# Optimization experiments

Hardware: AMD Instinct MI355X
Metric: run time of the kernel (lower is better)

## Reference

```python
import jax, jax.numpy as jnp
import numpy as np

B, S, D_IN, D_OUT = 4, 2048, 1024, 1024

def setup_inputs() -> dict:
    key = jax.random.key(0)
    k_x, k_q, k_k, k_v = jax.random.split(key, 4)
    return {
        "x": jax.random.normal(k_x, (B, S, D_IN), dtype=jnp.float32),
        "W_query": jax.random.uniform(k_q, (D_IN, D_OUT), dtype=jnp.float32),
        "W_key": jax.random.uniform(k_k, (D_IN, D_OUT), dtype=jnp.float32),
        "W_value": jax.random.uniform(k_v, (D_IN, D_OUT), dtype=jnp.float32),
    }

def reference(x, W_query, W_key, W_value):
    seq_len = x.shape[1]
    d_out = W_key.shape[-1]
    # fused QKV projection: x @ concat([Wq, Wk, Wv], -1), then split
    qkv = x @ jnp.concatenate([W_query, W_key, W_value], axis=-1)  # [B,S,3*d_out]
    query, key, value = jnp.split(qkv, 3, axis=2)
    # raw scores [B,S,S]; causal mask applied BEFORE scaling (as in source)
    attn_weights = jnp.einsum("bqd,bkd->bqk", query, key)
    causal = jnp.triu(jnp.ones((seq_len, seq_len), dtype=bool), k=1)
    attn_weights = jnp.where(causal[None, :, :], -jnp.inf, attn_weights)
    scaled = attn_weights / jnp.asarray(d_out, x.dtype) ** 0.5
    attn_scores = jax.nn.softmax(scaled, axis=-1)  # dropout p=0 -> identity
    context_vectors = jnp.einsum("bqk,bkd->bqd", attn_scores, value)
    return (context_vectors, attn_scores)
```

## Files before the change

### kernel.cpp

```cpp
#include <hip/hip_runtime.h>
#include <cstdint>
#include <cstddef>


#define S_LEN 2048
#define D_DIM 1024
#define NBATCH 4
#define MEG (1024 * 1024)

typedef __attribute__((ext_vector_type(4))) float floatx4;
typedef __attribute__((ext_vector_type(8))) __bf16 bf16x8;
typedef __attribute__((ext_vector_type(8))) short short8v;

__device__ __forceinline__ unsigned short f2bf(float f) {
  union { float f; unsigned u; } v; v.f = f;
  unsigned r = v.u + 0x7FFF + ((v.u >> 16) & 1);
  return (unsigned short)(r >> 16);
}
__device__ __forceinline__ float bf2f(unsigned short h) {
  union { unsigned u; float f; } v; v.u = ((unsigned)h) << 16; return v.f;
}

__device__ __forceinline__ void async_copy16(const void* g, void* l) {
  __builtin_amdgcn_global_load_lds(
      (const __attribute__((address_space(1))) void*)g,
      (__attribute__((address_space(3))) void*)l, 16, 0, 0);
}

#define VMCNT0() asm volatile("s_waitcnt vmcnt(0)" ::: "memory")
#define RAW_BAR() __builtin_amdgcn_s_barrier()
#define MFMA_BF16 __builtin_amdgcn_mfma_f32_16x16x32_bf16


__device__ __forceinline__ void split_core8_db(
    const short* __restrict__ Ah, const short* __restrict__ Al,
    const short* __restrict__ Bh, const short* __restrict__ Bl,
    int lda, int ldb, int kIters, int blockM, int blockN,
    short (*AsH)[256][32], short (*AsL)[256][32],
    short (*BsH)[128][32], short (*BsL)[128][32],
    floatx4 (&acc)[4][4])
{
  const int tid  = threadIdx.x;
  const int lane = tid & 63;
  const int wave = tid >> 6;
  const int wm = (wave >> 1) * 64;
  const int wn = (wave & 1) * 64;
  const int fm = lane & 15;
  const int fu = lane >> 4;

  int rA[4], sA[4], rB[4], sB[4];
  #pragma unroll
  for (int i = 0; i < 4; ++i) {
    rA[i] = wm + i * 16 + fm;
    sA[i] = (fu ^ ((rA[i] >> 1) & 3)) * 8;
    rB[i] = wn + i * 16 + fm;
    sB[i] = (fu ^ ((rB[i] >> 1) & 3)) * 8;
  }

  floatx4 zero = {0.f, 0.f, 0.f, 0.f};
  #pragma unroll
  for (int i = 0; i < 4; ++i)
    #pragma unroll
    for (int j = 0; j < 4; ++j)
      acc[i][j] = zero;

  const int r0 = tid >> 2;
  const int u0 = tid & 3;
  const int su = (u0 ^ ((r0 >> 1) & 3)) * 8;
  const size_t a0 = (size_t)(blockM + r0) * lda + su;
  const size_t a1 = a0 + (size_t)128 * lda;
  const size_t b0 = (size_t)(blockN + r0) * ldb + su;

  auto stage0 = [&](int bf, int kb) {
    async_copy16(Ah + a0 + kb, &AsH[bf][r0][u0 * 8]);
    async_copy16(Al + a0 + kb, &AsL[bf][r0][u0 * 8]);
    async_copy16(Bh + b0 + kb, &BsH[bf][r0][u0 * 8]);
  };
  auto stage1 = [&](int bf, int kb) {
    async_copy16(Ah + a1 + kb, &AsH[bf][r0 + 128][u0 * 8]);
    async_copy16(Al + a1 + kb, &AsL[bf][r0 + 128][u0 * 8]);
    async_copy16(Bl + b0 + kb, &BsL[bf][r0][u0 * 8]);
  };

  stage0(0, 0);
  stage1(0, 0);
  VMCNT0();
  RAW_BAR();

  for (int kt = 0; kt < kIters; ++kt) {
    const int cur = kt & 1;
    const int kb = (kt + 1) * 32;
    const bool pf = (kt + 1) < kIters;

    bf16x8 bh[4], bl[4];
    #pragma unroll
    for (int j = 0; j < 4; ++j) {
      bh[j] = *(const bf16x8*)(&BsH[cur][rB[j]][sB[j]]);
      bl[j] = *(const bf16x8*)(&BsL[cur][rB[j]][sB[j]]);
    }
    bf16x8 ah0 = *(const bf16x8*)(&AsH[cur][rA[0]][sA[0]]);
    bf16x8 al0 = *(const bf16x8*)(&AsL[cur][rA[0]][sA[0]]);
    bf16x8 ah1 = *(const bf16x8*)(&AsH[cur][rA[1]][sA[1]]);
    bf16x8 al1 = *(const bf16x8*)(&AsL[cur][rA[1]][sA[1]]);
    if (pf) stage0(cur ^ 1, kb);
    RAW_BAR();
    __builtin_amdgcn_s_setprio(1);
    #pragma unroll
    for (int j = 0; j < 4; ++j) {
      acc[0][j] = MFMA_BF16(ah0, bh[j], acc[0][j], 0, 0, 0);
      acc[0][j] = MFMA_BF16(ah0, bl[j], acc[0][j], 0, 0, 0);
      acc[0][j] = MFMA_BF16(al0, bh[j], acc[0][j], 0, 0, 0);
      acc[1][j] = MFMA_BF16(ah1, bh[j], acc[1][j], 0, 0, 0);
      acc[1][j] = MFMA_BF16(ah1, bl[j], acc[1][j], 0, 0, 0);
      acc[1][j] = MFMA_BF16(al1, bh[j], acc[1][j], 0, 0, 0);
    }
    __builtin_amdgcn_s_setprio(0);
    RAW_BAR();

    bf16x8 ah2 = *(const bf16x8*)(&AsH[cur][rA[2]][sA[2]]);
    bf16x8 al2 = *(const bf16x8*)(&AsL[cur][rA[2]][sA[2]]);
    bf16x8 ah3 = *(const bf16x8*)(&AsH[cur][rA[3]][sA[3]]);
    bf16x8 al3 = *(const bf16x8*)(&AsL[cur][rA[3]][sA[3]]);
    if (pf) stage1(cur ^ 1, kb);
    RAW_BAR();
    __builtin_amdgcn_s_setprio(1);
    #pragma unroll
    for (int j = 0; j < 4; ++j) {
      acc[2][j] = MFMA_BF16(ah2, bh[j], acc[2][j], 0, 0, 0);
      acc[2][j] = MFMA_BF16(ah2, bl[j], acc[2][j], 0, 0, 0);
      acc[2][j] = MFMA_BF16(al2, bh[j], acc[2][j], 0, 0, 0);
      acc[3][j] = MFMA_BF16(ah3, bh[j], acc[3][j], 0, 0, 0);
      acc[3][j] = MFMA_BF16(ah3, bl[j], acc[3][j], 0, 0, 0);
      acc[3][j] = MFMA_BF16(al3, bh[j], acc[3][j], 0, 0, 0);
    }
    __builtin_amdgcn_s_setprio(0);
    VMCNT0();
    RAW_BAR();
  }
}

__device__ __forceinline__ void split_core8_sb(
    const short* __restrict__ Ah, const short* __restrict__ Al,
    const short* __restrict__ Bh, const short* __restrict__ Bl,
    int lda, int ldb, int kIters, int blockM, int blockN,
    short (*AsH)[32], short (*AsL)[32],
    short (*BsH)[32], short (*BsL)[32],
    floatx4 (&acc)[4][4])
{
  const int tid  = threadIdx.x;
  const int lane = tid & 63;
  const int wave = tid >> 6;
  const int wm = (wave >> 1) * 64;
  const int wn = (wave & 1) * 64;
  const int fm = lane & 15;
  const int fu = lane >> 4;

  int rA[4], sA[4], rB[4], sB[4];
  #pragma unroll
  for (int i = 0; i < 4; ++i) {
    rA[i] = wm + i * 16 + fm;
    sA[i] = (fu ^ ((rA[i] >> 1) & 3)) * 8;
    rB[i] = wn + i * 16 + fm;
    sB[i] = (fu ^ ((rB[i] >> 1) & 3)) * 8;
  }

  floatx4 zero = {0.f, 0.f, 0.f, 0.f};
  #pragma unroll
  for (int i = 0; i < 4; ++i)
    #pragma unroll
    for (int j = 0; j < 4; ++j)
      acc[i][j] = zero;

  const int r0 = tid >> 2;
  const int u0 = tid & 3;
  const int su = (u0 ^ ((r0 >> 1) & 3)) * 8;
  const size_t a0 = (size_t)(blockM + r0) * lda + su;
  const size_t a1 = a0 + (size_t)128 * lda;
  const size_t b0 = (size_t)(blockN + r0) * ldb + su;

  for (int kt = 0; kt < kIters; ++kt) {
    const int kb = kt * 32;
    async_copy16(Ah + a0 + kb, &AsH[r0][u0 * 8]);
    async_copy16(Al + a0 + kb, &AsL[r0][u0 * 8]);
    async_copy16(Bh + b0 + kb, &BsH[r0][u0 * 8]);
    async_copy16(Ah + a1 + kb, &AsH[r0 + 128][u0 * 8]);
    async_copy16(Al + a1 + kb, &AsL[r0 + 128][u0 * 8]);
    async_copy16(Bl + b0 + kb, &BsL[r0][u0 * 8]);
    __syncthreads();

    bf16x8 bh[4], bl[4], ah[4], al[4];
    #pragma unroll
    for (int j = 0; j < 4; ++j) {
      bh[j] = *(const bf16x8*)(&BsH[rB[j]][sB[j]]);
      bl[j] = *(const bf16x8*)(&BsL[rB[j]][sB[j]]);
    }
    #pragma unroll
    for (int i = 0; i < 4; ++i) {
      ah[i] = *(const bf16x8*)(&AsH[rA[i]][sA[i]]);
      al[i] = *(const bf16x8*)(&AsL[rA[i]][sA[i]]);
    }
    __builtin_amdgcn_s_setprio(1);
    #pragma unroll
    for (int i = 0; i < 4; ++i)
      #pragma unroll
      for (int j = 0; j < 4; ++j) {
        acc[i][j] = MFMA_BF16(ah[i], bh[j], acc[i][j], 0, 0, 0);
        acc[i][j] = MFMA_BF16(ah[i], bl[j], acc[i][j], 0, 0, 0);
        acc[i][j] = MFMA_BF16(al[i], bh[j], acc[i][j], 0, 0, 0);
      }
    __builtin_amdgcn_s_setprio(0);
    __syncthreads();
  }
}

__device__ __forceinline__ void single_core8_sb(
    const short* __restrict__ A, const short* __restrict__ B,
    int lda, int ldb, int kIters, int blockM, int blockN,
    short (*As)[32], short (*Bs)[32], floatx4 (&acc)[4][4])
{
  const int tid  = threadIdx.x;
  const int lane = tid & 63;
  const int wave = tid >> 6;
  const int wm = (wave >> 1) * 64;
  const int wn = (wave & 1) * 64;
  const int fm = lane & 15;
  const int fu = lane >> 4;

  int rA[4], sA[4], rB[4], sB[4];
  #pragma unroll
  for (int i = 0; i < 4; ++i) {
    rA[i] = wm + i * 16 + fm;
    sA[i] = (fu ^ ((rA[i] >> 1) & 3)) * 8;
    rB[i] = wn + i * 16 + fm;
    sB[i] = (fu ^ ((rB[i] >> 1) & 3)) * 8;
  }

  floatx4 zero = {0.f, 0.f, 0.f, 0.f};
  #pragma unroll
  for (int i = 0; i < 4; ++i)
    #pragma unroll
    for (int j = 0; j < 4; ++j)
      acc[i][j] = zero;

  const int r0 = tid >> 2;
  const int u0 = tid & 3;
  const int su = (u0 ^ ((r0 >> 1) & 3)) * 8;
  const size_t a0 = (size_t)(blockM + r0) * lda + su;
  const size_t a1 = a0 + (size_t)128 * lda;
  const size_t b0 = (size_t)(blockN + r0) * ldb + su;

  for (int kt = 0; kt < kIters; ++kt) {
    const int kb = kt * 32;
    async_copy16(A + a0 + kb, &As[r0][u0 * 8]);
    async_copy16(B + b0 + kb, &Bs[r0][u0 * 8]);
    async_copy16(A + a1 + kb, &As[r0 + 128][u0 * 8]);
    __syncthreads();

    bf16x8 bfr[4], af[4];
    #pragma unroll
    for (int j = 0; j < 4; ++j)
      bfr[j] = *(const bf16x8*)(&Bs[rB[j]][sB[j]]);
    #pragma unroll
    for (int i = 0; i < 4; ++i)
      af[i] = *(const bf16x8*)(&As[rA[i]][sA[i]]);

    __builtin_amdgcn_s_setprio(1);
    #pragma unroll
    for (int i = 0; i < 4; ++i)
      #pragma unroll
      for (int j = 0; j < 4; ++j)
        acc[i][j] = MFMA_BF16(af[i], bfr[j], acc[i][j], 0, 0, 0);
    __builtin_amdgcn_s_setprio(0);
    __syncthreads();
  }
}


__global__ __launch_bounds__(256) void k_cvt_w(
    const float* __restrict__ wq, const float* __restrict__ wk,
    const float* __restrict__ wv,
    short* __restrict__ wqh, short* __restrict__ wql,
    short* __restrict__ wkh, short* __restrict__ wkl,
    short* __restrict__ wvt, float* __restrict__ muSum,
    int* __restrict__ cnt)
{
  const int bid = blockIdx.x;
  const int tid = threadIdx.x;
  if (bid < 1024) {
    const float4* src;
    short *dh, *dl;
    size_t idx;
    if (bid < 512) {
      idx = (size_t)bid * 256 + tid;
      src = (const float4*)wq; dh = wqh; dl = wql;
    } else {
      idx = (size_t)(bid - 512) * 256 + tid;
      src = (const float4*)wk; dh = wkh; dl = wkl;
    }
    const float4 u4 = src[idx * 2];
    const float4 w4 = src[idx * 2 + 1];
    float f[8] = {u4.x, u4.y, u4.z, u4.w, w4.x, w4.y, w4.z, w4.w};
    short8v oh, ol;
    #pragma unroll
    for (int e = 0; e < 8; ++e) {
      const unsigned short h = f2bf(f[e]);
      oh[e] = (short)h;
      ol[e] = (short)f2bf(f[e] - bf2f(h));
    }
    *(short8v*)(dh + idx * 8) = oh;
    *(short8v*)(dl + idx * 8) = ol;
  } else {
    if (bid == 1024) {
      float4 z = {0.f, 0.f, 0.f, 0.f};
      ((float4*)muSum)[tid] = z;
      if (tid == 0) *cnt = 0;
    }
    const int rem = bid - 1024;
    const int bx = rem & 31, by = rem >> 5;
    const int tx = tid & 31, ty = tid >> 5;
    __shared__ float tile[32][33];
    const int colIn = bx * 32 + tx;
    #pragma unroll
    for (int i = 0; i < 4; ++i) {
      const int rowIn = by * 32 + ty + i * 8;
      tile[ty + i * 8][tx] = wv[(size_t)rowIn * D_DIM + colIn];
    }
    __syncthreads();
    const int colOut = by * 32 + tx;
    #pragma unroll
    for (int i = 0; i < 4; ++i) {
      const int rowOut = bx * 32 + ty + i * 8;
      wvt[(size_t)rowOut * D_DIM + colOut] = (short)f2bf(tile[tx][ty + i * 8]);
    }
  }
}


__global__ __launch_bounds__(256) void k_m_cvtx(
    const short* __restrict__ wqh, const short* __restrict__ wql,
    const short* __restrict__ wkh, const short* __restrict__ wkl,
    short* __restrict__ mth, short* __restrict__ mtl,
    float* __restrict__ muSum,
    const float4* __restrict__ x,
    short* __restrict__ xh, short* __restrict__ xl)
{
  __shared__ alignas(16) short AsH[2][64][32];
  __shared__ alignas(16) short AsL[2][64][32];
  __shared__ alignas(16) short BsH[2][64][32];
  __shared__ alignas(16) short BsL[2][64][32];
  const int g = blockIdx.x;
  const int tid = threadIdx.x;

  if (g < 256) {
    floatx4 acc[2][2];
    const int blockM = (g >> 4) * 64;
    const int blockN = (g & 15) * 64;
    const int lane = tid & 63, wave = tid >> 6;
    const int wm = (wave >> 1) * 32, wn = (wave & 1) * 32;
    const int fm = lane & 15, fk = (lane >> 4) * 8;

    floatx4 zero = {0.f, 0.f, 0.f, 0.f};
    #pragma unroll
    for (int i = 0; i < 2; ++i)
      #pragma unroll
      for (int j = 0; j < 2; ++j)
        acc[i][j] = zero;

    const int sr = tid >> 2;
    const int sc = (tid & 3) * 8;
    const short* ah0 = wkh + (size_t)(blockM + sr) * D_DIM + sc;
    const short* al0 = wkl + (size_t)(blockM + sr) * D_DIM + sc;
    const short* bh0 = wqh + (size_t)(blockN + sr) * D_DIM + sc;
    const short* bl0 = wql + (size_t)(blockN + sr) * D_DIM + sc;
    short* ahB = &AsH[0][0][0]; short* alB = &AsL[0][0][0];
    short* bhB = &BsH[0][0][0]; short* blB = &BsL[0][0][0];
    const int l0 = tid * 8, l1 = (tid + 256) * 8;

    for (int kt = 0; kt < 16; ++kt) {
      const int kb = kt * 64;
      async_copy16(ah0 + kb, ahB + l0);
      async_copy16(ah0 + kb + 32, ahB + l1);
      async_copy16(al0 + kb, alB + l0);
      async_copy16(al0 + kb + 32, alB + l1);
      async_copy16(bh0 + kb, bhB + l0);
      async_copy16(bh0 + kb + 32, bhB + l1);
      async_copy16(bl0 + kb, blB + l0);
      async_copy16(bl0 + kb + 32, blB + l1);
      __syncthreads();
      #pragma unroll
      for (int ks = 0; ks < 2; ++ks) {
        bf16x8 ah[2], al[2], bh[2], bl[2];
        #pragma unroll
        for (int i = 0; i < 2; ++i) {
          ah[i] = *(const bf16x8*)(&AsH[ks][wm + i * 16 + fm][fk]);
          al[i] = *(const bf16x8*)(&AsL[ks][wm + i * 16 + fm][fk]);
        }
        #pragma unroll
        for (int j = 0; j < 2; ++j) {
          bh[j] = *(const bf16x8*)(&BsH[ks][wn + j * 16 + fm][fk]);
          bl[j] = *(const bf16x8*)(&BsL[ks][wn + j * 16 + fm][fk]);
        }
        #pragma unroll
        for (int i = 0; i < 2; ++i)
          #pragma unroll
          for (int j = 0; j < 2; ++j) {
            acc[i][j] = MFMA_BF16(ah[i], bh[j], acc[i][j], 0, 0, 0);
            acc[i][j] = MFMA_BF16(ah[i], bl[j], acc[i][j], 0, 0, 0);
            acc[i][j] = MFMA_BF16(al[i], bh[j], acc[i][j], 0, 0, 0);
          }
      }
      __syncthreads();
    }

    const int rb = wm + ((lane >> 4) << 2);
    const int cb = wn + (lane & 15);
    #pragma unroll
    for (int i = 0; i < 2; ++i)
      #pragma unroll
      for (int j = 0; j < 2; ++j) {
        const int n = blockN + cb + j * 16;
        #pragma unroll
        for (int r = 0; r < 2 * 2; ++r) {
          const int m = blockM + rb + i * 16 + r;
          const float f = acc[i][j][r];
          const unsigned short h = f2bf(f);
          mth[(size_t)m * D_DIM + n] = (short)h;
          mtl[(size_t)m * D_DIM + n] = (short)f2bf(f - bf2f(h));
        }
      }
    #pragma unroll
    for (int i = 0; i < 2; ++i)
      #pragma unroll
      for (int r = 0; r < 4; ++r) {
        float v = acc[i][0][r] + acc[i][1][r];
        v += __shfl_xor(v, 1); v += __shfl_xor(v, 2);
        v += __shfl_xor(v, 4); v += __shfl_xor(v, 8);
        if ((lane & 15) == 0)
          atomicAdd(&muSum[blockM + rb + i * 16 + r], v);
      }
  } else {
    const size_t idx = (size_t)(g - 256) * 256 + tid;
    const float4 u4 = x[idx * 2];
    const float4 w4 = x[idx * 2 + 1];
    float f[8] = {u4.x, u4.y, u4.z, u4.w, w4.x, w4.y, w4.z, w4.w};
    short8v oh, ol;
    #pragma unroll
    for (int e = 0; e < 8; ++e) {
      const unsigned short h = f2bf(f[e]);
      oh[e] = (short)h;
      ol[e] = (short)f2bf(f[e] - bf2f(h));
    }
    *(short8v*)(xh + idx * 8) = oh;
    *(short8v*)(xl + idx * 8) = ol;
  }
}


__global__ __launch_bounds__(256) void k_rowstats(
    const short* __restrict__ xh, const short* __restrict__ xl,
    const float* __restrict__ muSum, float* __restrict__ sq, float* __restrict__ u)
{
  const int r = blockIdx.x, tid = threadIdx.x;
  const ushort4 h = *(const ushort4*)(xh + (size_t)r * D_DIM + tid * 4);
  const ushort4 l = *(const ushort4*)(xl + (size_t)r * D_DIM + tid * 4);
  const float4 m4 = *(const float4*)(muSum + tid * 4);
  const float x0 = bf2f(h.x) + bf2f(l.x);
  const float x1 = bf2f(h.y) + bf2f(l.y);
  const float x2 = bf2f(h.z) + bf2f(l.z);
  const float x3 = bf2f(h.w) + bf2f(l.w);
  float s = x0 + x1 + x2 + x3;
  float uu = m4.x * x0 + m4.y * x1 + m4.z * x2 + m4.w * x3;
  #pragma unroll
  for (int off = 32; off > 0; off >>= 1) {
    s  += __shfl_xor(s, off);
    uu += __shfl_xor(uu, off);
  }
  __shared__ float ps[4], pu[4];
  if ((tid & 63) == 0) { ps[tid >> 6] = s; pu[tid >> 6] = uu; }
  __syncthreads();
  if (tid == 0) {
    sq[r] = ps[0] + ps[1] + ps[2] + ps[3];
    u[r]  = (pu[0] + pu[1] + pu[2] + pu[3]) * (1.0f / 1024.0f);
  }
}


__global__ __launch_bounds__(512) void k_gemm_n8(
    const short* __restrict__ xh, const short* __restrict__ xl,
    const short* __restrict__ mth, const short* __restrict__ mtl,
    const float* __restrict__ sq, const float* __restrict__ muSum,
    short* __restrict__ nh, short* __restrict__ nl)
{
  __shared__ alignas(16) short AsH[2][256][32];
  __shared__ alignas(16) short AsL[2][256][32];
  __shared__ alignas(16) short BsH[2][128][32];
  __shared__ alignas(16) short BsL[2][128][32];
  floatx4 acc[4][4];
  const int g = blockIdx.x;
  const int swz = (g & 7) * 32 + (g >> 3);
  const int blockM = (swz >> 3) * 256;
  const int blockN = (swz & 7) * 128;
  split_core8_db(xh, xl, mth, mtl, D_DIM, D_DIM, D_DIM / 32,
                 blockM, blockN, AsH, AsL, BsH, BsL, acc);

  const int tid = threadIdx.x, lane = tid & 63, wave = tid >> 6;
  const int wm = (wave >> 1) * 64, wn = (wave & 1) * 64;
  const int rb = wm + ((lane >> 4) << 2);
  const int cb = wn + (lane & 15);
  #pragma unroll
  for (int i = 0; i < 4; ++i)
    #pragma unroll
    for (int j = 0; j < 4; ++j) {
      const int n = blockN + cb + j * 16;
      const float muv = muSum[n] * (1.0f / 1024.0f);
      #pragma unroll
      for (int r = 0; r < 4; ++r) {
        const int m = blockM + rb + i * 16 + r;
        const float f = acc[i][j][r] - sq[m] * muv;
        const unsigned short h = f2bf(f);
        nh[(size_t)m * D_DIM + n] = (short)h;
        nl[(size_t)m * D_DIM + n] = (short)f2bf(f - bf2f(h));
      }
    }
}


__global__ __launch_bounds__(512) void k_gemm_sv8(
    const short* __restrict__ nh, const short* __restrict__ nl,
    const short* __restrict__ xh, const short* __restrict__ xl,
    const float* __restrict__ sq, const float* __restrict__ u,
    const short* __restrict__ wvt, float* __restrict__ attn,
    short* __restrict__ vt, int* __restrict__ cnt)
{
  __shared__ alignas(16) short AsH[256][32];
  __shared__ alignas(16) short AsL[256][32];
  __shared__ alignas(16) short BsH[128][32];
  __shared__ alignas(16) short BsL[128][32];
  __shared__ int s_item;

  const int tid = threadIdx.x, lane = tid & 63, wave = tid >> 6;
  const int wm = (wave >> 1) * 64, wn = (wave & 1) * 64;
  const int rb = wm + ((lane >> 4) << 2);
  const int cb = wn + (lane & 15);

  for (;;) {
    if (tid == 0) s_item = atomicAdd(cnt, 1);
    __syncthreads();
    const int item = s_item;
    if (item >= 544) return;

    floatx4 acc[4][4];
    if (item < 288) {
      const int b = item / 72;
      int t = item - b * 72;
      int bi = 0;
      while (t >= 2 * bi + 2) { t -= 2 * bi + 2; ++bi; }
      const int bj = t;

      const size_t boff = (size_t)b * S_LEN * D_DIM;
      split_core8_sb(nh + boff, nl + boff, xh + boff, xl + boff,
                     D_DIM, D_DIM, D_DIM / 32, bi * 256, bj * 128,
                     AsH, AsL, BsH, BsL, acc);

      float* out = attn + (size_t)b * S_LEN * S_LEN;
      const int rowBase = (b << 11) + bi * 256;
      const int colBase = (b << 11) + bj * 128;
      #pragma unroll
      for (int j = 0; j < 4; ++j) {
        const int n = bj * 128 + cb + j * 16;
        const float uv = u[colBase + cb + j * 16];
        #pragma unroll
        for (int i = 0; i < 4; ++i)
          #pragma unroll
          for (int r = 0; r < 4; ++r) {
            const int m = bi * 256 + rb + i * 16 + r;
            const float sv = sq[rowBase + rb + i * 16 + r];
            out[(size_t)m * S_LEN + n] = acc[i][j][r] + sv * uv;
          }
      }
    } else {
      const int vb = item - 288;
      const int blockM = (vb >> 3) * 256;
      const int blockN = (vb & 7) * 128;
      single_core8_sb(xh, wvt, D_DIM, D_DIM, D_DIM / 32, blockM, blockN,
                      AsH, BsH, acc);
      #pragma unroll
      for (int i = 0; i < 4; ++i)
        #pragma unroll
        for (int j = 0; j < 4; ++j) {
          const int n = blockN + cb + j * 16;
          const int m0 = blockM + rb + i * 16;
          const int b = m0 >> 11;
          const int s0 = m0 & (S_LEN - 1);
          ushort4 pk;
          pk.x = f2bf(acc[i][j][0]); pk.y = f2bf(acc[i][j][1]);
          pk.z = f2bf(acc[i][j][2]); pk.w = f2bf(acc[i][j][3]);
          *(ushort4*)(vt + ((size_t)b * D_DIM + n) * S_LEN + s0) = pk;
        }
    }
  }
}


__global__ __launch_bounds__(256) void k_softmax(float* __restrict__ attn,
                                                 short* __restrict__ pb) {
  const int b = blockIdx.x >> 11;
  const int q = blockIdx.x & (S_LEN - 1);
  float* row  = attn + ((size_t)b * S_LEN + q) * S_LEN;
  short* prow = pb   + ((size_t)b * S_LEN + q) * S_LEN;
  const int tid = threadIdx.x;
  const int k0 = tid * 8;
  const int kBand = ((q >> 7) + 1) << 7;
  __shared__ float sMax[4], sSum[4];

  float v[8];
  if (k0 <= q) {
    const float4 a0 = *(const float4*)(row + k0);
    const float4 a1 = *(const float4*)(row + k0 + 4);
    v[0] = a0.x; v[1] = a0.y; v[2] = a0.z; v[3] = a0.w;
    v[4] = a1.x; v[5] = a1.y; v[6] = a1.z; v[7] = a1.w;
  } else {
    #pragma unroll
    for (int e = 0; e < 8; ++e) v[e] = -3.0e38f;
  }

  float mx = -3.0e38f;
  #pragma unroll
  for (int e = 0; e < 8; ++e) {
    v[e] = (k0 + e <= q) ? v[e] : -3.0e38f;
    mx = fmaxf(mx, v[e]);
  }
  #pragma unroll
  for (int off = 32; off > 0; off >>= 1) mx = fmaxf(mx, __shfl_xor(mx, off));
  if ((tid & 63) == 0) sMax[tid >> 6] = mx;
  __syncthreads();
  mx = fmaxf(fmaxf(sMax[0], sMax[1]), fmaxf(sMax[2], sMax[3]));

  float s = 0.f;
  #pragma unroll
  for (int e = 0; e < 8; ++e) {
    const float p = (k0 + e <= q) ? __expf((v[e] - mx) * 0.03125f) : 0.f;
    v[e] = p;
    s += p;
  }
  #pragma unroll
  for (int off = 32; off > 0; off >>= 1) s += __shfl_xor(s, off);
  if ((tid & 63) == 0) sSum[tid >> 6] = s;
  __syncthreads();
  s = sSum[0] + sSum[1] + sSum[2] + sSum[3];
  const float inv = 1.0f / s;

  float o[8];
  #pragma unroll
  for (int e = 0; e < 8; ++e) o[e] = v[e] * inv;
  float4 w0 = {o[0], o[1], o[2], o[3]};
  float4 w1 = {o[4], o[5], o[6], o[7]};
  *(float4*)(row + k0) = w0;
  *(float4*)(row + k0 + 4) = w1;
  if (k0 < kBand) {
    ushort4 p0, p1;
    p0.x = f2bf(o[0]); p0.y = f2bf(o[1]); p0.z = f2bf(o[2]); p0.w = f2bf(o[3]);
    p1.x = f2bf(o[4]); p1.y = f2bf(o[5]); p1.z = f2bf(o[6]); p1.w = f2bf(o[7]);
    *(ushort4*)(prow + k0) = p0;
    *(ushort4*)(prow + k0 + 4) = p1;
  }
}


__global__ __launch_bounds__(256) void k_gemm_ctx(
    const short* __restrict__ pb, const short* __restrict__ vt,
    float* __restrict__ ctx)
{
  __shared__ alignas(16) short As2[2][128][32];
  __shared__ alignas(16) short Bs2[2][128][32];
  floatx4 acc[4][4];
  const int b = blockIdx.z;
  const int by = 15 - blockIdx.y;
  const int blockM = by * 128;
  const int blockN = blockIdx.x * 128;
  const int kIters = (by + 1) * 2;
  const short* A = pb + (size_t)b * S_LEN * S_LEN;
  const short* B = vt + (size_t)b * D_DIM * S_LEN;

  const int tid = threadIdx.x, lane = tid & 63, wave = tid >> 6;
  const int wm = (wave >> 1) * 64, wn = (wave & 1) * 64;
  const int fm = lane & 15, fk = (lane >> 4) * 8;
  const int r0 = tid >> 2, c0 = (tid & 3) * 8;

  floatx4 zero = {0.f, 0.f, 0.f, 0.f};
  #pragma unroll
  for (int i = 0; i < 4; ++i)
    #pragma unroll
    for (int j = 0; j < 4; ++j)
      acc[i][j] = zero;

  const short* a0 = A + (size_t)(blockM + r0) * S_LEN + c0;
  const short* a1 = a0 + (size_t)64 * S_LEN;
  const short* b0 = B + (size_t)(blockN + r0) * S_LEN + c0;
  const short* b1 = b0 + (size_t)64 * S_LEN;
  short* asBase = &As2[0][0][0];
  short* bsBase = &Bs2[0][0][0];
  short* as0 = asBase + (size_t)tid * 8;
  short* as1 = asBase + (size_t)(tid + 256) * 8;
  short* as2 = asBase + (size_t)(tid + 512) * 8;
  short* as3 = asBase + (size_t)(tid + 768) * 8;
  short* bs0 = bsBase + (size_t)tid * 8;
  short* bs1 = bsBase + (size_t)(tid + 256) * 8;
  short* bs2 = bsBase + (size_t)(tid + 512) * 8;
  short* bs3 = bsBase + (size_t)(tid + 768) * 8;

  for (int kt = 0; kt < kIters; ++kt) {
    const int kb = kt * 64;
    async_copy16(a0 + kb, as0);
    async_copy16(a1 + kb, as1);
    async_copy16(a0 + kb + 32, as2);
    async_copy16(a1 + kb + 32, as3);
    async_copy16(b0 + kb, bs0);
    async_copy16(b1 + kb, bs1);
    async_copy16(b0 + kb + 32, bs2);
    async_copy16(b1 + kb + 32, bs3);
    __syncthreads();
    #pragma unroll
    for (int ks = 0; ks < 2; ++ks) {
      bf16x8 af[4], bfr[4];
      #pragma unroll
      for (int i = 0; i < 4; ++i)
        af[i] = *(const bf16x8*)(&As2[ks][wm + i * 16 + fm][fk]);
      #pragma unroll
      for (int j = 0; j < 4; ++j)
        bfr[j] = *(const bf16x8*)(&Bs2[ks][wn + j * 16 + fm][fk]);
      #pragma unroll
      for (int i = 0; i < 4; ++i)
        #pragma unroll
        for (int j = 0; j < 4; ++j)
          acc[i][j] = MFMA_BF16(af[i], bfr[j], acc[i][j], 0, 0, 0);
    }
    __syncthreads();
  }

  float* out = ctx + (size_t)b * S_LEN * D_DIM;
  const int rb = wm + ((lane >> 4) << 2);
  const int cb = wn + (lane & 15);
  #pragma unroll
  for (int i = 0; i < 4; ++i)
    #pragma unroll
    for (int j = 0; j < 4; ++j) {
      const int n = blockN + cb + j * 16;
      #pragma unroll
      for (int r = 0; r < 4; ++r) {
        const int m = blockM + rb + i * 16 + r;
        out[(size_t)m * D_DIM + n] = acc[i][j][r];
      }
    }
}


extern "C" void kernel_launch(void* const* d_in, const int* in_sizes, int n_in,
                              void* d_out, int out_size, void* d_ws, size_t ws_size,
                              hipStream_t stream) {
  const float* x  = (const float*)d_in[0];
  const float* wq = (const float*)d_in[1];
  const float* wk = (const float*)d_in[2];
  const float* wv = (const float*)d_in[3];

  float* out  = (float*)d_out;
  float* ctx  = out;
  float* attn = out + (size_t)NBATCH * S_LEN * D_DIM;

  short* ws  = (short*)d_ws;
  short* xh  = ws;
  short* xl  = xh + (size_t)8 * MEG;
  short* wqh = xl + (size_t)8 * MEG;
  short* wql = wqh + (size_t)1 * MEG;
  short* wkh = wql + (size_t)1 * MEG;
  short* wkl = wkh + (size_t)1 * MEG;
  short* wvt = wkl + (size_t)1 * MEG;
  short* mth = wvt + (size_t)1 * MEG;
  short* mtl = mth + (size_t)1 * MEG;
  short* nh  = mtl + (size_t)1 * MEG;
  short* nl  = nh + (size_t)8 * MEG;
  short* vt  = nl + (size_t)8 * MEG;
  short* pb  = nh;
  float* fb  = (float*)(vt + (size_t)8 * MEG);
  float* muS = fb;
  float* sq  = fb + 1024;
  float* u   = sq + 8192;
  int*   cnt = (int*)(u + 8192);

  k_cvt_w<<<2048, 256, 0, stream>>>(wq, wk, wv, wqh, wql, wkh, wkl, wvt,
                                    muS, cnt);
  k_m_cvtx<<<4352, 256, 0, stream>>>(wqh, wql, wkh, wkl, mth, mtl, muS,
                                     (const float4*)x, xh, xl);
  k_rowstats<<<8192, 256, 0, stream>>>(xh, xl, muS, sq, u);
  k_gemm_n8<<<256, 512, 0, stream>>>(xh, xl, mth, mtl, sq, muS, nh, nl);
  k_gemm_sv8<<<512, 512, 0, stream>>>(nh, nl, xh, xl, sq, u, wvt, attn,
                                      vt, cnt);
  k_softmax<<<NBATCH * S_LEN, 256, 0, stream>>>(attn, pb);
  k_gemm_ctx<<<dim3(8, 16, 4), 256, 0, stream>>>(pb, vt, ctx);
}
```

Measured before the change: 376.4 us.

## Shrink split-bf16 GEMM tiles to 128x128 with 256-thread blocks and swizzle ctx LDS

The split-precision GEMM kernels move from 256x128 tiles on 512-thread blocks (one of them double-buffered) to 128x128 tiles on 256-thread single-buffered blocks with launch_bounds occupancy 3. The item counts and grids are rescaled so the causal-triangle scheduler covers finer tiles. This gives more blocks and better load balance on the causal triangle, at the cost of less operand reuse per tile and the loss of double buffering. The ctx GEMM also gains an XOR-swizzled LDS layout to cut bank conflicts, plus setprio around its MFMA blocks.

```diff
diff --git a/kernel.cpp b/kernel.cpp
--- a/kernel.cpp
+++ b/kernel.cpp
@@ -32,114 +32,7 @@
 #define MFMA_BF16 __builtin_amdgcn_mfma_f32_16x16x32_bf16
 
 
-__device__ __forceinline__ void split_core8_db(
-    const short* __restrict__ Ah, const short* __restrict__ Al,
-    const short* __restrict__ Bh, const short* __restrict__ Bl,
-    int lda, int ldb, int kIters, int blockM, int blockN,
-    short (*AsH)[256][32], short (*AsL)[256][32],
-    short (*BsH)[128][32], short (*BsL)[128][32],
-    floatx4 (&acc)[4][4])
-{
-  const int tid  = threadIdx.x;
-  const int lane = tid & 63;
-  const int wave = tid >> 6;
-  const int wm = (wave >> 1) * 64;
-  const int wn = (wave & 1) * 64;
-  const int fm = lane & 15;
-  const int fu = lane >> 4;
-
-  int rA[4], sA[4], rB[4], sB[4];
-  #pragma unroll
-  for (int i = 0; i < 4; ++i) {
-    rA[i] = wm + i * 16 + fm;
-    sA[i] = (fu ^ ((rA[i] >> 1) & 3)) * 8;
-    rB[i] = wn + i * 16 + fm;
-    sB[i] = (fu ^ ((rB[i] >> 1) & 3)) * 8;
-  }
-
-  floatx4 zero = {0.f, 0.f, 0.f, 0.f};
-  #pragma unroll
-  for (int i = 0; i < 4; ++i)
-    #pragma unroll
-    for (int j = 0; j < 4; ++j)
-      acc[i][j] = zero;
-
-  const int r0 = tid >> 2;
-  const int u0 = tid & 3;
-  const int su = (u0 ^ ((r0 >> 1) & 3)) * 8;
-  const size_t a0 = (size_t)(blockM + r0) * lda + su;
-  const size_t a1 = a0 + (size_t)128 * lda;
-  const size_t b0 = (size_t)(blockN + r0) * ldb + su;
-
-  auto stage0 = [&](int bf, int kb) {
-    async_copy16(Ah + a0 + kb, &AsH[bf][r0][u0 * 8]);
-    async_copy16(Al + a0 + kb, &AsL[bf][r0][u0 * 8]);
-    async_copy16(Bh + b0 + kb, &BsH[bf][r0][u0 * 8]);
-  };
-  auto stage1 = [&](int bf, int kb) {
-    async_copy16(Ah + a1 + kb, &AsH[bf][r0 + 128][u0 * 8]);
-    async_copy16(Al + a1 + kb, &AsL[bf][r0 + 128][u0 * 8]);
-    async_copy16(Bl + b0 + kb, &BsL[bf][r0][u0 * 8]);
-  };
-
-  stage0(0, 0);
-  stage1(0, 0);
-  VMCNT0();
-  RAW_BAR();
-
-  for (int kt = 0; kt < kIters; ++kt) {
-    const int cur = kt & 1;
-    const int kb = (kt + 1) * 32;
-    const bool pf = (kt + 1) < kIters;
-
-    bf16x8 bh[4], bl[4];
-    #pragma unroll
-    for (int j = 0; j < 4; ++j) {
-      bh[j] = *(const bf16x8*)(&BsH[cur][rB[j]][sB[j]]);
-      bl[j] = *(const bf16x8*)(&BsL[cur][rB[j]][sB[j]]);
-    }
-    bf16x8 ah0 = *(const bf16x8*)(&AsH[cur][rA[0]][sA[0]]);
-    bf16x8 al0 = *(const bf16x8*)(&AsL[cur][rA[0]][sA[0]]);
-    bf16x8 ah1 = *(const bf16x8*)(&AsH[cur][rA[1]][sA[1]]);
-    bf16x8 al1 = *(const bf16x8*)(&AsL[cur][rA[1]][sA[1]]);
-    if (pf) stage0(cur ^ 1, kb);
-    RAW_BAR();
-    __builtin_amdgcn_s_setprio(1);
-    #pragma unroll
-    for (int j = 0; j < 4; ++j) {
-      acc[0][j] = MFMA_BF16(ah0, bh[j], acc[0][j], 0, 0, 0);
-      acc[0][j] = MFMA_BF16(ah0, bl[j], acc[0][j], 0, 0, 0);
-      acc[0][j] = MFMA_BF16(al0, bh[j], acc[0][j], 0, 0, 0);
-      acc[1][j] = MFMA_BF16(ah1, bh[j], acc[1][j], 0, 0, 0);
-      acc[1][j] = MFMA_BF16(ah1, bl[j], acc[1][j], 0, 0, 0);
-      acc[1][j] = MFMA_BF16(al1, bh[j], acc[1][j], 0, 0, 0);
-    }
-    __builtin_amdgcn_s_setprio(0);
-    RAW_BAR();
-
-    bf16x8 ah2 = *(const bf16x8*)(&AsH[cur][rA[2]][sA[2]]);
-    bf16x8 al2 = *(const bf16x8*)(&AsL[cur][rA[2]][sA[2]]);
-    bf16x8 ah3 = *(const bf16x8*)(&AsH[cur][rA[3]][sA[3]]);
-    bf16x8 al3 = *(const bf16x8*)(&AsL[cur][rA[3]][sA[3]]);
-    if (pf) stage1(cur ^ 1, kb);
-    RAW_BAR();
-    __builtin_amdgcn_s_setprio(1);
-    #pragma unroll
-    for (int j = 0; j < 4; ++j) {
-      acc[2][j] = MFMA_BF16(ah2, bh[j], acc[2][j], 0, 0, 0);
-      acc[2][j] = MFMA_BF16(ah2, bl[j], acc[2][j], 0, 0, 0);
-      acc[2][j] = MFMA_BF16(al2, bh[j], acc[2][j], 0, 0, 0);
-      acc[3][j] = MFMA_BF16(ah3, bh[j], acc[3][j], 0, 0, 0);
-      acc[3][j] = MFMA_BF16(ah3, bl[j], acc[3][j], 0, 0, 0);
-      acc[3][j] = MFMA_BF16(al3, bh[j], acc[3][j], 0, 0, 0);
-    }
-    __builtin_amdgcn_s_setprio(0);
-    VMCNT0();
-    RAW_BAR();
-  }
-}
-
-__device__ __forceinline__ void split_core8_sb(
+__device__ __forceinline__ void split_core4(
     const short* __restrict__ Ah, const short* __restrict__ Al,
     const short* __restrict__ Bh, const short* __restrict__ Bl,
     int lda, int ldb, int kIters, int blockM, int blockN,
@@ -175,17 +68,20 @@
   const int u0 = tid & 3;
   const int su = (u0 ^ ((r0 >> 1) & 3)) * 8;
   const size_t a0 = (size_t)(blockM + r0) * lda + su;
-  const size_t a1 = a0 + (size_t)128 * lda;
+  const size_t a1 = a0 + (size_t)64 * lda;
   const size_t b0 = (size_t)(blockN + r0) * ldb + su;
+  const size_t b1 = b0 + (size_t)64 * ldb;
 
   for (int kt = 0; kt < kIters; ++kt) {
     const int kb = kt * 32;
     async_copy16(Ah + a0 + kb, &AsH[r0][u0 * 8]);
+    async_copy16(Ah + a1 + kb, &AsH[r0 + 64][u0 * 8]);
     async_copy16(Al + a0 + kb, &AsL[r0][u0 * 8]);
+    async_copy16(Al + a1 + kb, &AsL[r0 + 64][u0 * 8]);
     async_copy16(Bh + b0 + kb, &BsH[r0][u0 * 8]);
-    async_copy16(Ah + a1 + kb, &AsH[r0 + 128][u0 * 8]);
-    async_copy16(Al + a1 + kb, &AsL[r0 + 128][u0 * 8]);
+    async_copy16(Bh + b1 + kb, &BsH[r0 + 64][u0 * 8]);
     async_copy16(Bl + b0 + kb, &BsL[r0][u0 * 8]);
+    async_copy16(Bl + b1 + kb, &BsL[r0 + 64][u0 * 8]);
     __syncthreads();
 
     bf16x8 bh[4], bl[4], ah[4], al[4];
@@ -213,7 +109,7 @@
   }
 }
 
-__device__ __forceinline__ void single_core8_sb(
+__device__ __forceinline__ void single_core4(
     const short* __restrict__ A, const short* __restrict__ B,
     int lda, int ldb, int kIters, int blockM, int blockN,
     short (*As)[32], short (*Bs)[32], floatx4 (&acc)[4][4])
@@ -246,14 +142,16 @@
   const int u0 = tid & 3;
   const int su = (u0 ^ ((r0 >> 1) & 3)) * 8;
   const size_t a0 = (size_t)(blockM + r0) * lda + su;
-  const size_t a1 = a0 + (size_t)128 * lda;
+  const size_t a1 = a0 + (size_t)64 * lda;
   const size_t b0 = (size_t)(blockN + r0) * ldb + su;
+  const size_t b1 = b0 + (size_t)64 * ldb;
 
   for (int kt = 0; kt < kIters; ++kt) {
     const int kb = kt * 32;
     async_copy16(A + a0 + kb, &As[r0][u0 * 8]);
+    async_copy16(A + a1 + kb, &As[r0 + 64][u0 * 8]);
     async_copy16(B + b0 + kb, &Bs[r0][u0 * 8]);
-    async_copy16(A + a1 + kb, &As[r0 + 128][u0 * 8]);
+    async_copy16(B + b1 + kb, &Bs[r0 + 64][u0 * 8]);
     __syncthreads();
 
     bf16x8 bfr[4], af[4];
@@ -485,23 +383,23 @@
 }
 
 
-__global__ __launch_bounds__(512) void k_gemm_n8(
+__global__ __launch_bounds__(256, 3) void k_gemm_n4(
     const short* __restrict__ xh, const short* __restrict__ xl,
     const short* __restrict__ mth, const short* __restrict__ mtl,
     const float* __restrict__ sq, const float* __restrict__ muSum,
     short* __restrict__ nh, short* __restrict__ nl)
 {
-  __shared__ alignas(16) short AsH[2][256][32];
-  __shared__ alignas(16) short AsL[2][256][32];
-  __shared__ alignas(16) short BsH[2][128][32];
-  __shared__ alignas(16) short BsL[2][128][32];
+  __shared__ alignas(16) short AsH[128][32];
+  __shared__ alignas(16) short AsL[128][32];
+  __shared__ alignas(16) short BsH[128][32];
+  __shared__ alignas(16) short BsL[128][32];
   floatx4 acc[4][4];
   const int g = blockIdx.x;
-  const int swz = (g & 7) * 32 + (g >> 3);
-  const int blockM = (swz >> 3) * 256;
+  const int swz = (g & 7) * 64 + (g >> 3);
+  const int blockM = (swz >> 3) * 128;
   const int blockN = (swz & 7) * 128;
-  split_core8_db(xh, xl, mth, mtl, D_DIM, D_DIM, D_DIM / 32,
-                 blockM, blockN, AsH, AsL, BsH, BsL, acc);
+  split_core4(xh, xl, mth, mtl, D_DIM, D_DIM, D_DIM / 32,
+              blockM, blockN, AsH, AsL, BsH, BsL, acc);
 
   const int tid = threadIdx.x, lane = tid & 63, wave = tid >> 6;
   const int wm = (wave >> 1) * 64, wn = (wave & 1) * 64;
@@ -525,15 +423,15 @@
 }
 
 
-__global__ __launch_bounds__(512) void k_gemm_sv8(
+__global__ __launch_bounds__(256, 3) void k_gemm_sv4(
     const short* __restrict__ nh, const short* __restrict__ nl,
     const short* __restrict__ xh, const short* __restrict__ xl,
     const float* __restrict__ sq, const float* __restrict__ u,
     const short* __restrict__ wvt, float* __restrict__ attn,
     short* __restrict__ vt, int* __restrict__ cnt)
 {
-  __shared__ alignas(16) short AsH[256][32];
-  __shared__ alignas(16) short AsL[256][32];
+  __shared__ alignas(16) short AsH[128][32];
+  __shared__ alignas(16) short AsL[128][32];
   __shared__ alignas(16) short BsH[128][32];
   __shared__ alignas(16) short BsL[128][32];
   __shared__ int s_item;
@@ -547,23 +445,23 @@
     if (tid == 0) s_item = atomicAdd(cnt, 1);
     __syncthreads();
     const int item = s_item;
-    if (item >= 544) return;
+    if (item >= 1056) return;
 
     floatx4 acc[4][4];
-    if (item < 288) {
-      const int b = item / 72;
-      int t = item - b * 72;
+    if (item < 544) {
+      const int b = item / 136;
+      int t = item - b * 136;
       int bi = 0;
-      while (t >= 2 * bi + 2) { t -= 2 * bi + 2; ++bi; }
+      while (t >= bi + 1) { t -= bi + 1; ++bi; }
       const int bj = t;
 
       const size_t boff = (size_t)b * S_LEN * D_DIM;
-      split_core8_sb(nh + boff, nl + boff, xh + boff, xl + boff,
-                     D_DIM, D_DIM, D_DIM / 32, bi * 256, bj * 128,
-                     AsH, AsL, BsH, BsL, acc);
+      split_core4(nh + boff, nl + boff, xh + boff, xl + boff,
+                  D_DIM, D_DIM, D_DIM / 32, bi * 128, bj * 128,
+                  AsH, AsL, BsH, BsL, acc);
 
       float* out = attn + (size_t)b * S_LEN * S_LEN;
-      const int rowBase = (b << 11) + bi * 256;
+      const int rowBase = (b << 11) + bi * 128;
       const int colBase = (b << 11) + bj * 128;
       #pragma unroll
       for (int j = 0; j < 4; ++j) {
@@ -573,17 +471,17 @@
         for (int i = 0; i < 4; ++i)
           #pragma unroll
           for (int r = 0; r < 4; ++r) {
-            const int m = bi * 256 + rb + i * 16 + r;
+            const int m = bi * 128 + rb + i * 16 + r;
             const float sv = sq[rowBase + rb + i * 16 + r];
             out[(size_t)m * S_LEN + n] = acc[i][j][r] + sv * uv;
           }
       }
     } else {
-      const int vb = item - 288;
-      const int blockM = (vb >> 3) * 256;
+      const int vb = item - 544;
+      const int blockM = (vb >> 3) * 128;
       const int blockN = (vb & 7) * 128;
-      single_core8_sb(xh, wvt, D_DIM, D_DIM, D_DIM / 32, blockM, blockN,
-                      AsH, BsH, acc);
+      single_core4(xh, wvt, D_DIM, D_DIM, D_DIM / 32, blockM, blockN,
+                   AsH, BsH, acc);
       #pragma unroll
       for (int i = 0; i < 4; ++i)
         #pragma unroll
@@ -684,8 +582,17 @@
 
   const int tid = threadIdx.x, lane = tid & 63, wave = tid >> 6;
   const int wm = (wave >> 1) * 64, wn = (wave & 1) * 64;
-  const int fm = lane & 15, fk = (lane >> 4) * 8;
-  const int r0 = tid >> 2, c0 = (tid & 3) * 8;
+  const int fm = lane & 15;
+  const int fu = lane >> 4;
+
+  int rA[4], sA[4], rB[4], sB[4];
+  #pragma unroll
+  for (int i = 0; i < 4; ++i) {
+    rA[i] = wm + i * 16 + fm;
+    sA[i] = (fu ^ ((rA[i] >> 1) & 3)) * 8;
+    rB[i] = wn + i * 16 + fm;
+    sB[i] = (fu ^ ((rB[i] >> 1) & 3)) * 8;
+  }
 
   floatx4 zero = {0.f, 0.f, 0.f, 0.f};
   #pragma unroll
@@ -694,9 +601,12 @@
     for (int j = 0; j < 4; ++j)
       acc[i][j] = zero;
 
-  const short* a0 = A + (size_t)(blockM + r0) * S_LEN + c0;
+  const int r0 = tid >> 2;
+  const int u0 = tid & 3;
+  const int su = (u0 ^ ((r0 >> 1) & 3)) * 8;
+  const short* a0 = A + (size_t)(blockM + r0) * S_LEN + su;
   const short* a1 = a0 + (size_t)64 * S_LEN;
-  const short* b0 = B + (size_t)(blockN + r0) * S_LEN + c0;
+  const short* b0 = B + (size_t)(blockN + r0) * S_LEN + su;
   const short* b1 = b0 + (size_t)64 * S_LEN;
   short* asBase = &As2[0][0][0];
   short* bsBase = &Bs2[0][0][0];
@@ -725,15 +635,17 @@
       bf16x8 af[4], bfr[4];
       #pragma unroll
       for (int i = 0; i < 4; ++i)
-        af[i] = *(const bf16x8*)(&As2[ks][wm + i * 16 + fm][fk]);
+        af[i] = *(const bf16x8*)(&As2[ks][rA[i]][sA[i]]);
       #pragma unroll
       for (int j = 0; j < 4; ++j)
-        bfr[j] = *(const bf16x8*)(&Bs2[ks][wn + j * 16 + fm][fk]);
+        bfr[j] = *(const bf16x8*)(&Bs2[ks][rB[j]][sB[j]]);
+      __builtin_amdgcn_s_setprio(1);
       #pragma unroll
       for (int i = 0; i < 4; ++i)
         #pragma unroll
         for (int j = 0; j < 4; ++j)
           acc[i][j] = MFMA_BF16(af[i], bfr[j], acc[i][j], 0, 0, 0);
+      __builtin_amdgcn_s_setprio(0);
     }
     __syncthreads();
   }
@@ -792,8 +704,8 @@
   k_m_cvtx<<<4352, 256, 0, stream>>>(wqh, wql, wkh, wkl, mth, mtl, muS,
                                      (const float4*)x, xh, xl);
   k_rowstats<<<8192, 256, 0, stream>>>(xh, xl, muS, sq, u);
-  k_gemm_n8<<<256, 512, 0, stream>>>(xh, xl, mth, mtl, sq, muS, nh, nl);
-  k_gemm_sv8<<<512, 512, 0, stream>>>(nh, nl, xh, xl, sq, u, wvt, attn,
+  k_gemm_n4<<<512, 256, 0, stream>>>(xh, xl, mth, mtl, sq, muS, nh, nl);
+  k_gemm_sv4<<<768, 256, 0, stream>>>(nh, nl, xh, xl, sq, u, wvt, attn,
                                       vt, cnt);
   k_softmax<<<NBATCH * S_LEN, 256, 0, stream>>>(attn, pb);
   k_gemm_ctx<<<dim3(8, 16, 4), 256, 0, stream>>>(pb, vt, ctx);
```

Result: faster. 367.0 us (-2.5%).
